# Kernel tuning notes

Measured on AMD Instinct MI355X. Metric: run time of the kernel, lower is better.

The kernel has to match this reference:

```python
import jax, jax.numpy as jnp
import numpy as np

C_IN = 512
NUM_HEADS = 8
D_K = 64
D_V = 64


def setup_inputs() -> dict:
    key = jax.random.key(0)
    ks = jax.random.split(key, 6)
    scale = 1.0 / np.sqrt(C_IN)
    return {
        "x": jax.random.normal(ks[0], (8, C_IN, 32, 32), dtype=jnp.float32),
        "Wq": jax.random.normal(ks[1], (C_IN, NUM_HEADS * D_K), dtype=jnp.float32) * scale,
        "bq": jnp.zeros((NUM_HEADS * D_K,), dtype=jnp.float32),
        "Wk": jax.random.normal(ks[2], (C_IN, NUM_HEADS * D_K), dtype=jnp.float32) * scale,
        "bk": jnp.zeros((NUM_HEADS * D_K,), dtype=jnp.float32),
        "Wv": jax.random.normal(ks[3], (C_IN, NUM_HEADS * D_V), dtype=jnp.float32) * scale,
        "bv": jnp.zeros((NUM_HEADS * D_V,), dtype=jnp.float32),
        "Wo": jax.random.normal(ks[4], (NUM_HEADS * D_V, C_IN), dtype=jnp.float32) * scale,
        "bo": jnp.zeros((C_IN,), dtype=jnp.float32),
        "num_heads": NUM_HEADS,
    }


def reference(x, Wq, bq, Wk, bk, Wv, bv, Wo, bo, num_heads):
    B, C, H, W = x.shape
    S = H * W
    xs = x.reshape(B, C, S).transpose(0, 2, 1)  # [B, S, C]

    def split_heads(t):  # [B, S, nh*d] -> [B, nh, S, d]
        return t.reshape(B, S, num_heads, -1).transpose(0, 2, 1, 3)

    q = split_heads(xs @ Wq + bq)  # [B, nh, S, d_k]
    k = split_heads(xs @ Wk + bk)  # [B, nh, S, d_k]
    v = split_heads(xs @ Wv + bv)  # [B, nh, S, d_v]

    d_k = q.shape[-1]
    scores = jnp.einsum("bhqd,bhkd->bhqk", q, k) / jnp.sqrt(jnp.float32(d_k))
    probs = jax.nn.softmax(scores, axis=-1)
    attn = jnp.einsum("bhqk,bhkd->bhqd", probs, v)  # [B, nh, S, d_v]

    out = attn.transpose(0, 2, 1, 3).reshape(B, S, -1)  # [B, S, nh*d_v]
    out = out @ Wo + bo  # [B, S, C]
    out = out + xs  # residual
    return out.transpose(0, 2, 1).reshape(B, C, H, W)
```

## Files before the change

### kernel.cpp

```cpp
#include <hip/hip_runtime.h>

#define S_LEN 1024
#define CIN 512
#define NH 8
#define DH 64
#define NB 8

typedef short bf16x8 __attribute__((ext_vector_type(8)));
typedef float f32x4 __attribute__((ext_vector_type(4)));
typedef unsigned short u16x4 __attribute__((ext_vector_type(4)));

__device__ inline unsigned short f2bf(float f){
  union { float f; unsigned u; } v; v.f = f;
  unsigned r = v.u + 0x7FFFu + ((v.u >> 16) & 1u);
  return (unsigned short)(r >> 16);
}

__device__ inline void gload16(const void* g, void* l){
  __builtin_amdgcn_global_load_lds(
      (const __attribute__((address_space(1))) unsigned*)g,
      (__attribute__((address_space(3))) unsigned*)l, 16, 0, 0);
}

__device__ inline bf16x8 ldfrag(const unsigned short* lds, int row, int kbyte){
  return *(const bf16x8*)((const char*)lds + row*128 + (kbyte ^ ((row & 7) << 4)));
}

__global__ __launch_bounds__(256) void prep(const float* __restrict__ x,
    const float* __restrict__ Wq, const float* __restrict__ Wk,
    const float* __restrict__ Wv, const float* __restrict__ Wo,
    unsigned short* __restrict__ xs, unsigned short* __restrict__ Wqkt,
    unsigned short* __restrict__ Wvt, unsigned short* __restrict__ Wot){
  __shared__ unsigned short T[64*72];
  int bid = blockIdx.x, t = threadIdx.x;
  const float* src; unsigned short* dst; int ldS, r0, c0;
  if (bid < 1024){
    int b = bid >> 7, tt = bid & 127;
    src = x + (size_t)b*CIN*S_LEN; ldS = S_LEN;
    dst = xs + (size_t)b*S_LEN*CIN;
    r0 = (tt >> 4) * 64;
    c0 = (tt & 15) * 64;
  } else {
    int w = bid - 1024, mat = w >> 6, tt = w & 63;
    r0 = (tt >> 3) * 64; c0 = (tt & 7) * 64; ldS = 512;
    if (mat == 0){ src = Wq; dst = Wqkt; }
    else if (mat == 1){ src = Wk; dst = Wqkt + 512*512; }
    else if (mat == 2){ src = Wv; dst = Wvt; }
    else            { src = Wo; dst = Wot; }
  }
  int rl = t >> 4, cb = (t & 15) * 4;
  #pragma unroll
  for (int rr = 0; rr < 4; rr++){
    float4 f = *(const float4*)(src + (size_t)(r0 + rl + rr*16)*ldS + c0 + cb);
    int rc = rl + rr*16;
    T[(cb+0)*72 + rc] = f2bf(f.x);
    T[(cb+1)*72 + rc] = f2bf(f.y);
    T[(cb+2)*72 + rc] = f2bf(f.z);
    T[(cb+3)*72 + rc] = f2bf(f.w);
  }
  __syncthreads();
  int cl = t >> 2, rb = (t & 3) * 16;
  uint4 v0 = *(const uint4*)&T[cl*72 + rb];
  uint4 v1 = *(const uint4*)&T[cl*72 + rb + 8];
  *(uint4*)(dst + (size_t)(c0 + cl)*512 + r0 + rb) = v0;
  *(uint4*)(dst + (size_t)(c0 + cl)*512 + r0 + rb + 8) = v1;
}

__device__ inline void gemm128(const unsigned short* A, const unsigned short* B,
    unsigned short* As, unsigned short* Bs, f32x4 acc[4][4], int tid){
  int lane = tid & 63, w = tid >> 6;
  int wr = w >> 1, wc = w & 1;
  int srow = lane >> 3;
  int scol8 = ((lane & 7) ^ (lane >> 3)) << 3;
  for (int k0 = 0; k0 < 512; k0 += 64){
    __syncthreads();
    #pragma unroll
    for (int i = 0; i < 4; i++){
      int r0 = w*32 + i*8;
      gload16(A + (size_t)(r0 + srow)*512 + k0 + scol8, As + r0*64);
      gload16(B + (size_t)(r0 + srow)*512 + k0 + scol8, Bs + r0*64);
    }
    __syncthreads();
    #pragma unroll
    for (int kt = 0; kt < 2; kt++){
      bf16x8 af[4], bfv[4];
      #pragma unroll
      for (int i = 0; i < 4; i++){
        af[i]  = ldfrag(As, wr*64 + i*16 + (lane & 15), kt*64 + ((lane >> 4) << 4));
        bfv[i] = ldfrag(Bs, wc*64 + i*16 + (lane & 15), kt*64 + ((lane >> 4) << 4));
      }
      #pragma unroll
      for (int mi = 0; mi < 4; mi++)
        #pragma unroll
        for (int ni = 0; ni < 4; ni++)
          acc[mi][ni] = __builtin_amdgcn_mfma_f32_16x16x32_bf16(af[mi], bfv[ni], acc[mi][ni], 0,0,0);
    }
  }
}

__global__ __launch_bounds__(256) void qkv128(const unsigned short* __restrict__ xs,
    const unsigned short* __restrict__ Wqkt, const unsigned short* __restrict__ Wvt,
    const float* __restrict__ bq, const float* __restrict__ bk,
    const float* __restrict__ bv, unsigned short* __restrict__ q_ws,
    unsigned short* __restrict__ k_ws, unsigned short* __restrict__ vt_ws){
  __shared__ __align__(16) unsigned short As[8192], Bs[8192];
  int tid = threadIdx.x, lane = tid & 63, w = tid >> 6, wr = w >> 1, wc = w & 1;
  int bx = blockIdx.x, by = blockIdx.y, b = blockIdx.z;
  f32x4 acc[4][4];
  #pragma unroll
  for (int i = 0; i < 4; i++)
    #pragma unroll
    for (int j = 0; j < 4; j++) acc[i][j] = (f32x4){0.f,0.f,0.f,0.f};
  if (by < 8){
    int m0 = bx * 128, n0 = by * 128;
    gemm128(xs + (size_t)b*S_LEN*CIN + (size_t)m0*512, Wqkt + (size_t)n0*512, As, Bs, acc, tid);
    int jb = (n0 + wc*64) >> 6;
    int isK = jb >= 8, h = jb & 7;
    const float* bias = isK ? bk : bq;
    unsigned short* dst = (isK ? k_ws : q_ws) + ((size_t)(b*NH + h))*S_LEN*DH;
    #pragma unroll
    for (int nt = 0; nt < 4; nt++){
      int d = nt*16 + (lane & 15);
      float bb = bias[(jb & 7)*64 + d];
      #pragma unroll
      for (int mi = 0; mi < 4; mi++)
        #pragma unroll
        for (int r = 0; r < 4; r++){
          int s = m0 + wr*64 + mi*16 + (lane >> 4)*4 + r;
          dst[(size_t)s*DH + d] = f2bf(acc[mi][nt][r] + bb);
        }
    }
  } else {
    int m0 = (by - 8) * 128, n0 = bx * 128;
    gemm128(Wvt + (size_t)m0*512, xs + (size_t)b*S_LEN*CIN + (size_t)n0*512, As, Bs, acc, tid);
    #pragma unroll
    for (int mi = 0; mi < 4; mi++)
      #pragma unroll
      for (int r = 0; r < 4; r++){
        int j = m0 + wr*64 + mi*16 + (lane >> 4)*4 + r;
        int h = j >> 6, dv = j & 63;
        float bb = bv[j];
        unsigned short* dst = vt_ws + ((size_t)(b*NH + h)*DH + dv)*S_LEN;
        #pragma unroll
        for (int nt = 0; nt < 4; nt++){
          int s = n0 + wc*64 + nt*16 + (lane & 15);
          dst[s] = f2bf(acc[mi][nt][r] + bb);
        }
      }
  }
}

__global__ __launch_bounds__(256) void attn_fwd(const unsigned short* __restrict__ qw,
    const unsigned short* __restrict__ kw, const unsigned short* __restrict__ vtw,
    unsigned short* __restrict__ aw){
  __shared__ __align__(16) unsigned short Ks[4096], Vs[4096], Ps[4096];
  int tid = threadIdx.x, lane = tid & 63, wid = tid >> 6;
  int bid = blockIdx.x;
  int idx = bid >> 3, qb = idx & 15, bh = (bid & 7)*8 + (idx >> 4);
  int qrw = lane & 15, g = lane >> 4;
  int q0 = qb*64 + wid*16;
  const unsigned short* qrow = qw + ((size_t)bh*S_LEN + q0 + qrw)*DH;
  bf16x8 qf0 = *(const bf16x8*)(qrow + g*8);
  bf16x8 qf1 = *(const bf16x8*)(qrow + 32 + g*8);
  unsigned short* myP = Ps + wid*1024;
  f32x4 oacc[4];
  #pragma unroll
  for (int i = 0; i < 4; i++) oacc[i] = (f32x4){0.f,0.f,0.f,0.f};
  float mrun = -3e38f, lrun = 0.f;
  int srow = lane >> 3, scol8 = ((lane & 7) ^ (lane >> 3)) << 3;
  const unsigned short* kbase = kw + (size_t)bh*S_LEN*DH;
  const unsigned short* vbase = vtw + (size_t)bh*DH*S_LEN;
  const float SC = 0.125f * 1.44269504f;

  for (int kv0 = 0; kv0 < S_LEN; kv0 += 64){
    __syncthreads();
    #pragma unroll
    for (int i = 0; i < 2; i++){
      int r0 = wid*16 + i*8;
      gload16(kbase + (size_t)(kv0 + r0 + srow)*DH + scol8, Ks + r0*64);
      gload16(vbase + (size_t)(r0 + srow)*S_LEN + kv0 + scol8, Vs + r0*64);
    }
    __syncthreads();

    f32x4 st[4];
    #pragma unroll
    for (int mt = 0; mt < 4; mt++){
      f32x4 a = (f32x4){0.f,0.f,0.f,0.f};
      a = __builtin_amdgcn_mfma_f32_16x16x32_bf16(
            ldfrag(Ks, mt*16 + qrw, g << 4), qf0, a, 0,0,0);
      a = __builtin_amdgcn_mfma_f32_16x16x32_bf16(
            ldfrag(Ks, mt*16 + qrw, 64 + (g << 4)), qf1, a, 0,0,0);
      st[mt] = a;
    }
    float vmax = -3e38f;
    #pragma unroll
    for (int mt = 0; mt < 4; mt++)
      #pragma unroll
      for (int r = 0; r < 4; r++){
        st[mt][r] *= SC;
        vmax = fmaxf(vmax, st[mt][r]);
      }
    vmax = fmaxf(vmax, __shfl_xor(vmax, 16));
    vmax = fmaxf(vmax, __shfl_xor(vmax, 32));
    float mnew = fmaxf(mrun, vmax);
    float corr = __builtin_amdgcn_exp2f(mrun - mnew);
    float psum = 0.f;
    #pragma unroll
    for (int mt = 0; mt < 4; mt++){
      float p0 = __builtin_amdgcn_exp2f(st[mt][0] - mnew);
      float p1 = __builtin_amdgcn_exp2f(st[mt][1] - mnew);
      float p2 = __builtin_amdgcn_exp2f(st[mt][2] - mnew);
      float p3 = __builtin_amdgcn_exp2f(st[mt][3] - mnew);
      psum += (p0 + p1) + (p2 + p3);
      u16x4 w; w[0]=f2bf(p0); w[1]=f2bf(p1); w[2]=f2bf(p2); w[3]=f2bf(p3);
      *(u16x4*)((char*)myP + qrw*128 + ((mt*32 + g*8) ^ ((qrw & 7) << 4))) = w;
    }
    psum += __shfl_xor(psum, 16);
    psum += __shfl_xor(psum, 32);
    lrun = lrun * corr + psum;
    mrun = mnew;
    #pragma unroll
    for (int mt = 0; mt < 4; mt++) oacc[mt] *= corr;
    #pragma unroll
    for (int kt = 0; kt < 2; kt++){
      bf16x8 pf = *(const bf16x8*)((char*)myP + qrw*128 +
                    ((kt*64 + (g << 4)) ^ ((qrw & 7) << 4)));
      #pragma unroll
      for (int mt = 0; mt < 4; mt++)
        oacc[mt] = __builtin_amdgcn_mfma_f32_16x16x32_bf16(
            ldfrag(Vs, mt*16 + qrw, kt*64 + (g << 4)), pf, oacc[mt], 0,0,0);
    }
  }
  float inv = 1.f / lrun;
  #pragma unroll
  for (int mt = 0; mt < 4; mt++)
    #pragma unroll
    for (int r = 0; r < 4; r++){
      int dv = mt*16 + g*4 + r;
      *(unsigned short*)((char*)myP + qrw*128 + ((dv*2) ^ ((qrw & 7) << 4))) =
          f2bf(oacc[mt][r] * inv);
    }
  int b = bh >> 3, h = bh & 7;
  int rr = lane >> 2, cc = lane & 3;
  uint4 lo = *(const uint4*)((char*)myP + rr*128 + ((cc*32) ^ ((rr & 7) << 4)));
  uint4 hi = *(const uint4*)((char*)myP + rr*128 + (((cc*32) + 16) ^ ((rr & 7) << 4)));
  unsigned short* obase = aw + ((size_t)b*S_LEN + (q0 + rr))*512 + h*64 + cc*16;
  *(uint4*)obase = lo;
  *(uint4*)(obase + 8) = hi;
}

__global__ __launch_bounds__(256) void out128(const unsigned short* __restrict__ Wot,
    const unsigned short* __restrict__ aw, const float* __restrict__ bo,
    const float* __restrict__ x, float* __restrict__ out){
  __shared__ __align__(16) unsigned short As[8192], Bs[8192];
  int tid = threadIdx.x, lane = tid & 63, w = tid >> 6, wr = w >> 1, wc = w & 1;
  int m0 = blockIdx.x * 128, n0 = blockIdx.y * 128, b = blockIdx.z;
  f32x4 acc[4][4];
  #pragma unroll
  for (int i = 0; i < 4; i++)
    #pragma unroll
    for (int j = 0; j < 4; j++) acc[i][j] = (f32x4){0.f,0.f,0.f,0.f};
  gemm128(Wot + (size_t)m0*512, aw + (size_t)b*S_LEN*512 + (size_t)n0*512, As, Bs, acc, tid);
  #pragma unroll
  for (int mi = 0; mi < 4; mi++)
    #pragma unroll
    for (int r = 0; r < 4; r++){
      int c = m0 + wr*64 + mi*16 + (lane >> 4)*4 + r;
      float bb = bo[c];
      size_t rowb = ((size_t)b*CIN + c)*S_LEN;
      #pragma unroll
      for (int nt = 0; nt < 4; nt++){
        int s = n0 + wc*64 + nt*16 + (lane & 15);
        out[rowb + s] = acc[mi][nt][r] + bb + x[rowb + s];
      }
    }
}

extern "C" void kernel_launch(void* const* d_in, const int* in_sizes, int n_in,
                              void* d_out, int out_size, void* d_ws, size_t ws_size,
                              hipStream_t stream){
  const float* x  = (const float*)d_in[0];
  const float* Wq = (const float*)d_in[1];
  const float* bq = (const float*)d_in[2];
  const float* Wk = (const float*)d_in[3];
  const float* bk = (const float*)d_in[4];
  const float* Wv = (const float*)d_in[5];
  const float* bv = (const float*)d_in[6];
  const float* Wo = (const float*)d_in[7];
  const float* bo = (const float*)d_in[8];
  float* out = (float*)d_out;

  unsigned short* p = (unsigned short*)d_ws;
  const size_t xs_e   = (size_t)NB*S_LEN*CIN;
  const size_t qkv_e  = (size_t)NB*NH*S_LEN*DH;
  unsigned short* xs    = p;                 p += xs_e;
  unsigned short* Wqkt  = p;                 p += 1024*512;
  unsigned short* Wvt   = p;                 p += 512*512;
  unsigned short* Wot   = p;                 p += 512*512;
  unsigned short* q_ws  = p;                 p += qkv_e;
  unsigned short* k_ws  = p;                 p += qkv_e;
  unsigned short* vt_ws = p;                 p += qkv_e;
  unsigned short* aw    = p;                 p += qkv_e;

  prep<<<1280, 256, 0, stream>>>(x, Wq, Wk, Wv, Wo, xs, Wqkt, Wvt, Wot);
  qkv128<<<dim3(8, 12, NB), 256, 0, stream>>>(xs, Wqkt, Wvt, bq, bk, bv, q_ws, k_ws, vt_ws);
  attn_fwd<<<1024, 256, 0, stream>>>(q_ws, k_ws, vt_ws, aw);
  out128<<<dim3(4, 8, NB), 256, 0, stream>>>(Wot, aw, bo, x, out);
}
```

Baseline: 163.4 us.

## Double-buffer K/V tiles in attention, widen blocks to 8 waves, pack bf16 conversions

```diff
diff --git a/kernel.cpp b/kernel.cpp
--- a/kernel.cpp
+++ b/kernel.cpp
@@ -14,6 +14,12 @@
   union { float f; unsigned u; } v; v.f = f;
   unsigned r = v.u + 0x7FFFu + ((v.u >> 16) & 1u);
   return (unsigned short)(r >> 16);
+}
+
+__device__ inline unsigned cvt_pk_bf16(float a, float b){
+  unsigned r;
+  asm("v_cvt_pk_bf16_f32 %0, %1, %2" : "=v"(r) : "v"(a), "v"(b));
+  return r;
 }
 
 __device__ inline void gload16(const void* g, void* l){
@@ -150,15 +156,17 @@
   }
 }
 
-__global__ __launch_bounds__(256) void attn_fwd(const unsigned short* __restrict__ qw,
+__global__ __launch_bounds__(512) void attn_fwd(const unsigned short* __restrict__ qw,
     const unsigned short* __restrict__ kw, const unsigned short* __restrict__ vtw,
     unsigned short* __restrict__ aw){
-  __shared__ __align__(16) unsigned short Ks[4096], Vs[4096], Ps[4096];
+  __shared__ __align__(16) unsigned short Ks[2][4096], Vs[2][4096], Ps[8192];
   int tid = threadIdx.x, lane = tid & 63, wid = tid >> 6;
   int bid = blockIdx.x;
-  int idx = bid >> 3, qb = idx & 15, bh = (bid & 7)*8 + (idx >> 4);
+  int idx = bid >> 3;
+  int qb = idx & 7;
+  int bh = (bid & 7)*8 + (idx >> 3);
   int qrw = lane & 15, g = lane >> 4;
-  int q0 = qb*64 + wid*16;
+  int q0 = qb*128 + wid*16;
   const unsigned short* qrow = qw + ((size_t)bh*S_LEN + q0 + qrw)*DH;
   bf16x8 qf0 = *(const bf16x8*)(qrow + g*8);
   bf16x8 qf1 = *(const bf16x8*)(qrow + 32 + g*8);
@@ -171,25 +179,28 @@
   const unsigned short* kbase = kw + (size_t)bh*S_LEN*DH;
   const unsigned short* vbase = vtw + (size_t)bh*DH*S_LEN;
   const float SC = 0.125f * 1.44269504f;
+  int r0 = wid*8;
+  gload16(kbase + (size_t)(r0 + srow)*DH + scol8, Ks[0] + r0*64);
+  gload16(vbase + (size_t)(r0 + srow)*S_LEN + scol8, Vs[0] + r0*64);
+  __syncthreads();
+  int cur = 0;
 
   for (int kv0 = 0; kv0 < S_LEN; kv0 += 64){
-    __syncthreads();
-    #pragma unroll
-    for (int i = 0; i < 2; i++){
-      int r0 = wid*16 + i*8;
-      gload16(kbase + (size_t)(kv0 + r0 + srow)*DH + scol8, Ks + r0*64);
-      gload16(vbase + (size_t)(r0 + srow)*S_LEN + kv0 + scol8, Vs + r0*64);
-    }
-    __syncthreads();
+    if (kv0 + 64 < S_LEN){
+      gload16(kbase + (size_t)(kv0 + 64 + r0 + srow)*DH + scol8, Ks[cur^1] + r0*64);
+      gload16(vbase + (size_t)(r0 + srow)*S_LEN + kv0 + 64 + scol8, Vs[cur^1] + r0*64);
+    }
+    const unsigned short* Kc = Ks[cur];
+    const unsigned short* Vc = Vs[cur];
 
     f32x4 st[4];
     #pragma unroll
     for (int mt = 0; mt < 4; mt++){
       f32x4 a = (f32x4){0.f,0.f,0.f,0.f};
       a = __builtin_amdgcn_mfma_f32_16x16x32_bf16(
-            ldfrag(Ks, mt*16 + qrw, g << 4), qf0, a, 0,0,0);
+            ldfrag(Kc, mt*16 + qrw, g << 4), qf0, a, 0,0,0);
       a = __builtin_amdgcn_mfma_f32_16x16x32_bf16(
-            ldfrag(Ks, mt*16 + qrw, 64 + (g << 4)), qf1, a, 0,0,0);
+            ldfrag(Kc, mt*16 + qrw, 64 + (g << 4)), qf1, a, 0,0,0);
       st[mt] = a;
     }
     float vmax = -3e38f;
@@ -212,8 +223,8 @@
       float p2 = __builtin_amdgcn_exp2f(st[mt][2] - mnew);
       float p3 = __builtin_amdgcn_exp2f(st[mt][3] - mnew);
       psum += (p0 + p1) + (p2 + p3);
-      u16x4 w; w[0]=f2bf(p0); w[1]=f2bf(p1); w[2]=f2bf(p2); w[3]=f2bf(p3);
-      *(u16x4*)((char*)myP + qrw*128 + ((mt*32 + g*8) ^ ((qrw & 7) << 4))) = w;
+      uint2 pw; pw.x = cvt_pk_bf16(p0, p1); pw.y = cvt_pk_bf16(p2, p3);
+      *(uint2*)((char*)myP + qrw*128 + ((mt*32 + g*8) ^ ((qrw & 7) << 4))) = pw;
     }
     psum += __shfl_xor(psum, 16);
     psum += __shfl_xor(psum, 32);
@@ -228,18 +239,19 @@
       #pragma unroll
       for (int mt = 0; mt < 4; mt++)
         oacc[mt] = __builtin_amdgcn_mfma_f32_16x16x32_bf16(
-            ldfrag(Vs, mt*16 + qrw, kt*64 + (g << 4)), pf, oacc[mt], 0,0,0);
-    }
+            ldfrag(Vc, mt*16 + qrw, kt*64 + (g << 4)), pf, oacc[mt], 0,0,0);
+    }
+    __syncthreads();
+    cur ^= 1;
   }
   float inv = 1.f / lrun;
   #pragma unroll
-  for (int mt = 0; mt < 4; mt++)
-    #pragma unroll
-    for (int r = 0; r < 4; r++){
-      int dv = mt*16 + g*4 + r;
-      *(unsigned short*)((char*)myP + qrw*128 + ((dv*2) ^ ((qrw & 7) << 4))) =
-          f2bf(oacc[mt][r] * inv);
-    }
+  for (int mt = 0; mt < 4; mt++){
+    uint2 pw;
+    pw.x = cvt_pk_bf16(oacc[mt][0] * inv, oacc[mt][1] * inv);
+    pw.y = cvt_pk_bf16(oacc[mt][2] * inv, oacc[mt][3] * inv);
+    *(uint2*)((char*)myP + qrw*128 + ((mt*32 + g*8) ^ ((qrw & 7) << 4))) = pw;
+  }
   int b = bh >> 3, h = bh & 7;
   int rr = lane >> 2, cc = lane & 3;
   uint4 lo = *(const uint4*)((char*)myP + rr*128 + ((cc*32) ^ ((rr & 7) << 4)));
@@ -304,6 +316,6 @@
 
   prep<<<1280, 256, 0, stream>>>(x, Wq, Wk, Wv, Wo, xs, Wqkt, Wvt, Wot);
   qkv128<<<dim3(8, 12, NB), 256, 0, stream>>>(xs, Wqkt, Wvt, bq, bk, bv, q_ws, k_ws, vt_ws);
-  attn_fwd<<<1024, 256, 0, stream>>>(q_ws, k_ws, vt_ws, aw);
+  attn_fwd<<<512, 512, 0, stream>>>(q_ws, k_ws, vt_ws, aw);
   out128<<<dim3(4, 8, NB), 256, 0, stream>>>(Wot, aw, bo, x, out);
 }
```

Result: faster. 156.5 us (-4.2%).
